# Performance work log

Hardware: AMD Instinct MI355X
Metric: run time of the kernel (lower is better)

## Reference

```python
import jax, jax.numpy as jnp
import numpy as np

D_MODEL = 1024
N_HEADS = 16
N_GROUPS = 4
CONTEXT_LEN = 512
D_H = D_MODEL // N_HEADS          # 64
GROUP_SIZE = N_HEADS // N_GROUPS  # 4
B, S = 4, 2048


def setup_inputs() -> dict:
    key = jax.random.key(0)
    ks = jax.random.split(key, 9)
    s = 0.02
    return {
        "x": jax.random.normal(ks[0], (B, S, D_MODEL), dtype=jnp.float32),
        "Wq": jax.random.normal(ks[1], (D_MODEL, D_MODEL), dtype=jnp.float32) * s,
        "bq": jax.random.normal(ks[2], (D_MODEL,), dtype=jnp.float32) * s,
        "Wk": jax.random.normal(ks[3], (D_MODEL, N_GROUPS * D_H), dtype=jnp.float32) * s,
        "bk": jax.random.normal(ks[4], (N_GROUPS * D_H,), dtype=jnp.float32) * s,
        "Wv": jax.random.normal(ks[5], (D_MODEL, N_GROUPS * D_H), dtype=jnp.float32) * s,
        "bv": jax.random.normal(ks[6], (N_GROUPS * D_H,), dtype=jnp.float32) * s,
        "Wo": jax.random.normal(ks[7], (D_MODEL, D_MODEL), dtype=jnp.float32) * s,
        "bo": jax.random.normal(ks[8], (D_MODEL,), dtype=jnp.float32) * s,
    }


def reference(x, Wq, bq, Wk, bk, Wv, bv, Wo, bo):
    b, s = x.shape[0], x.shape[1]
    # Projections. q: [b, n_groups, group_size, s, d_h]; k/v: [b, n_groups, s, d_h]
    q = (x @ Wq + bq).reshape(b, s, N_GROUPS, GROUP_SIZE, D_H)
    q = jnp.transpose(q, (0, 2, 3, 1, 4))
    k = jnp.transpose((x @ Wk + bk).reshape(b, s, N_GROUPS, D_H), (0, 2, 1, 3))
    v = jnp.transpose((x @ Wv + bv).reshape(b, s, N_GROUPS, D_H), (0, 2, 1, 3))
    # Grouped scores (einsum broadcast == repeat_interleave of k over group_size)
    scores = jnp.einsum("bghqd,bgkd->bghqk", q, k) / jnp.sqrt(jnp.float32(D_H))
    # Sliding-window causal mask (cached_len == s when use_cache=False)
    i = jnp.arange(s)
    j = jnp.arange(s)
    upper = (i - CONTEXT_LEN)[:, None] >= j[None, :]   # too-old keys
    lower = i[:, None] < j[None, :]                    # future keys
    mask = upper | lower                               # [s, s]
    scores = jnp.where(mask, jnp.float32(-1e9), scores)
    att = jax.nn.softmax(scores, axis=-1)
    out = jnp.einsum("bghqk,bgkd->bghqd", att, v)      # [b, g, h, s, d_h]
    out = jnp.transpose(out, (0, 3, 1, 2, 4)).reshape(b, s, D_MODEL)
    return out @ Wo + bo
```

## Files before the change

kernel.cpp:

```cpp
#include <hip/hip_runtime.h>
#include <cstdint>
#include <cstddef>

typedef __attribute__((ext_vector_type(8))) short short8;
typedef __attribute__((ext_vector_type(4))) short short4v;
typedef __attribute__((ext_vector_type(4))) float f32x4;
typedef __attribute__((ext_vector_type(4))) unsigned short ushort4v;
typedef unsigned short ushort_t;

union PFrag { unsigned int w[4]; short8 v; };

__device__ __forceinline__ ushort_t f2bf(float f) {
  unsigned int u = __builtin_bit_cast(unsigned int, f);
  u += 0x7FFFu + ((u >> 16) & 1u);
  return (ushort_t)(u >> 16);
}

__device__ __forceinline__ void gload16(const void* g, void* l) {
  __builtin_amdgcn_global_load_lds(
      (const __attribute__((address_space(1))) unsigned int*)g,
      (__attribute__((address_space(3))) unsigned int*)l, 16, 0, 0);
}

__global__ __launch_bounds__(256) void prep_kernel(
    const float* __restrict__ x, ushort_t* __restrict__ xb,
    const float* __restrict__ Wq, const float* __restrict__ Wk,
    const float* __restrict__ Wv, const float* __restrict__ Wo,
    const float* __restrict__ bq, const float* __restrict__ bk,
    const float* __restrict__ bv, ushort_t* __restrict__ Wt,
    float* __restrict__ bqkv) {
  __shared__ float tile[32][33];
  const int t = threadIdx.x;
  if (blockIdx.x < 8192) {
    const int i = (blockIdx.x * 256 + t) * 4;
    const float4 v = *reinterpret_cast<const float4*>(x + i);
    ushort4v r = { f2bf(v.x), f2bf(v.y), f2bf(v.z), f2bf(v.w) };
    *reinterpret_cast<ushort4v*>(xb + i) = r;
    return;
  }
  const int bid = blockIdx.x - 8192;
  const int tn = bid % 80, tk = bid / 80;
  if (tk == 0) {
    const int u = tn * 256 + t;
    if (u < 1536) bqkv[u] = (u < 1024) ? bq[u] : (u < 1280) ? bk[u - 1024] : bv[u - 1280];
  }
  const int n0 = tn * 32;
  const float* W; int ldn, nloc;
  if      (n0 < 1024) { W = Wq; ldn = 1024; nloc = n0; }
  else if (n0 < 1280) { W = Wk; ldn = 256;  nloc = n0 - 1024; }
  else if (n0 < 1536) { W = Wv; ldn = 256;  nloc = n0 - 1280; }
  else                { W = Wo; ldn = 1024; nloc = n0 - 1536; }
  const int sr = t >> 3, sc = (t & 7) * 4;
  const float4 v = *reinterpret_cast<const float4*>(W + (size_t)(tk * 32 + sr) * ldn + nloc + sc);
  tile[sr][sc] = v.x; tile[sr][sc + 1] = v.y; tile[sr][sc + 2] = v.z; tile[sr][sc + 3] = v.w;
  __syncthreads();
  const int wr = t >> 3, wc = (t & 7) * 4;
  ushort4v o = { f2bf(tile[wc][wr]), f2bf(tile[wc + 1][wr]),
                 f2bf(tile[wc + 2][wr]), f2bf(tile[wc + 3][wr]) };
  *reinterpret_cast<ushort4v*>(Wt + (size_t)(n0 + wr) * 1024 + tk * 32 + wc) = o;
}

#define GEMM_IDS \
  const int tid = threadIdx.x;                        \
  const int w = tid >> 6, lane = tid & 63;            \
  const int wm = w >> 1, wn = w & 1;                  \
  const int g = lane >> 4, r16 = lane & 15;

#define GEMM_KLOOP(APTR, BPTR)                                                          \
  const f32x4 vzero = {0.f, 0.f, 0.f, 0.f};                                             \
  f32x4 acc[4][4];                                                                      \
  _Pragma("unroll") for (int i = 0; i < 4; ++i)                                         \
    _Pragma("unroll") for (int j = 0; j < 4; ++j) acc[i][j] = vzero;                    \
  auto stage = [&](int s, int k0) {                                                     \
    char* base = LdsB + s * 16384;                                                      \
    _Pragma("unroll") for (int i = 0; i < 2; ++i) {                                     \
      const int u = tid + i * 256;                                                      \
      const int row = u >> 2;                                                           \
      const int pu = (u & 3) ^ ((u >> 3) & 3);                                          \
      gload16((const char*)(APTR) + (size_t)(bm * 128 + row) * 2048 + k0 * 2 + pu * 16, \
              base + u * 16);                                                           \
    }                                                                                   \
    _Pragma("unroll") for (int i = 0; i < 2; ++i) {                                     \
      const int u = tid + i * 256;                                                      \
      const int row = u >> 2;                                                           \
      const int pu = (u & 3) ^ ((u >> 3) & 3);                                          \
      gload16((const char*)(BPTR) + (size_t)(bn * 128 + row) * 2048 + k0 * 2 + pu * 16, \
              base + 8192 + u * 16);                                                    \
    }                                                                                   \
  };                                                                                    \
  stage(0, 0);                                                                          \
  stage(1, 32);                                                                         \
  stage(2, 64);                                                                         \
  const int fsw = (g ^ ((r16 >> 1) & 3)) << 4;                                          \
  for (int t = 0; t < 32; ++t) {                                                        \
    if (t < 30)      { asm volatile("s_waitcnt vmcnt(8) lgkmcnt(0)" ::: "memory"); }    \
    else if (t == 30){ asm volatile("s_waitcnt vmcnt(4) lgkmcnt(0)" ::: "memory"); }    \
    else             { asm volatile("s_waitcnt vmcnt(0) lgkmcnt(0)" ::: "memory"); }    \
    __builtin_amdgcn_s_barrier();                                                       \
    if (t + 3 < 32) stage((t + 3) & 3, (t + 3) * 32);                                   \
    const char* Ab = LdsB + (t & 3) * 16384;                                            \
    const char* Bb = Ab + 8192;                                                         \
    short8 af[4], bf[4];                                                                \
    _Pragma("unroll") for (int mi = 0; mi < 4; ++mi)                                    \
      af[mi] = *(const short8*)(Ab + (wm * 64 + mi * 16 + r16) * 64 + fsw);             \
    _Pragma("unroll") for (int ni = 0; ni < 4; ++ni)                                    \
      bf[ni] = *(const short8*)(Bb + (wn * 64 + ni * 16 + r16) * 64 + fsw);             \
    __builtin_amdgcn_s_setprio(1);                                                      \
    _Pragma("unroll") for (int mi = 0; mi < 4; ++mi)                                    \
      _Pragma("unroll") for (int ni = 0; ni < 4; ++ni)                                  \
        acc[mi][ni] = __builtin_amdgcn_mfma_f32_16x16x32_bf16(af[mi], bf[ni], acc[mi][ni], 0, 0, 0); \
    __builtin_amdgcn_s_setprio(0);                                                      \
  }

__global__ __launch_bounds__(256, 2) void gemm_qkv_kernel(
    const ushort_t* __restrict__ A, const ushort_t* __restrict__ Bt,
    const float* __restrict__ bias,
    ushort_t* __restrict__ Qb, ushort_t* __restrict__ Kb, ushort_t* __restrict__ Vt)
{
  __shared__ __align__(16) char LdsB[65536];
  const int xcd = blockIdx.x & 7, ii = blockIdx.x >> 3;
  const int bm = xcd * 8 + ii / 12, bn = ii % 12;
  GEMM_IDS
  GEMM_KLOOP(A, Bt)

  float bcol[4];
#pragma unroll
  for (int ni = 0; ni < 4; ++ni) bcol[ni] = bias[bn * 128 + wn * 64 + ni * 16 + r16];
  if (bn < 8) {
#pragma unroll
    for (int mi = 0; mi < 4; ++mi)
#pragma unroll
      for (int ni = 0; ni < 4; ++ni) {
        const int col = bn * 128 + wn * 64 + ni * 16 + r16;
#pragma unroll
        for (int rr = 0; rr < 4; ++rr) {
          const int row = bm * 128 + wm * 64 + mi * 16 + g * 4 + rr;
          Qb[(size_t)row * 1024 + col] = f2bf((acc[mi][ni][rr] + bcol[ni]) * 0.180336881f);
        }
      }
  } else if (bn < 10) {
#pragma unroll
    for (int mi = 0; mi < 4; ++mi)
#pragma unroll
      for (int ni = 0; ni < 4; ++ni) {
        const int c = bn * 128 + wn * 64 + ni * 16 + r16 - 1024;
        const int gi = c >> 6, dd = c & 63;
#pragma unroll
        for (int rr = 0; rr < 4; ++rr) {
          const int row = bm * 128 + wm * 64 + mi * 16 + g * 4 + rr;
          const int bb = row >> 11, s = row & 2047;
          Kb[((size_t)(bb * 4 + gi) * 2048 + s) * 64 + dd] = f2bf(acc[mi][ni][rr] + bcol[ni]);
        }
      }
  } else {
#pragma unroll
    for (int mi = 0; mi < 4; ++mi) {
      const int row0 = bm * 128 + wm * 64 + mi * 16 + g * 4;
      const int bb = row0 >> 11;
      const int s = row0 & 2047;
      const int pos = (s & ~31) + g * 8 + (mi & 1) * 4;
#pragma unroll
      for (int ni = 0; ni < 4; ++ni) {
        const int c = bn * 128 + wn * 64 + ni * 16 + r16 - 1280;
        const int gi = c >> 6, dd = c & 63;
        ushort4v pk;
#pragma unroll
        for (int rr = 0; rr < 4; ++rr) pk[rr] = f2bf(acc[mi][ni][rr] + bcol[ni]);
        *reinterpret_cast<ushort4v*>(Vt + ((size_t)(bb * 4 + gi) * 64 + dd) * 2048 + pos) = pk;
      }
    }
  }
}

__global__ __launch_bounds__(256, 2) void gemm_out_kernel(
    const ushort_t* __restrict__ A, const ushort_t* __restrict__ Bt,
    const float* __restrict__ bias, float* __restrict__ Cout)
{
  __shared__ __align__(16) char LdsB[65536];
  const int xcd = blockIdx.x & 7, ii = blockIdx.x >> 3;
  const int bm = xcd * 8 + (ii >> 3), bn = ii & 7;
  GEMM_IDS
  GEMM_KLOOP(A, Bt)

  float bcol[4];
#pragma unroll
  for (int ni = 0; ni < 4; ++ni) bcol[ni] = bias[bn * 128 + wn * 64 + ni * 16 + r16];
#pragma unroll
  for (int mi = 0; mi < 4; ++mi)
#pragma unroll
    for (int ni = 0; ni < 4; ++ni) {
      const int col = bn * 128 + wn * 64 + ni * 16 + r16;
#pragma unroll
      for (int rr = 0; rr < 4; ++rr) {
        const int row = bm * 128 + wm * 64 + mi * 16 + g * 4 + rr;
        Cout[(size_t)row * 1024 + col] = acc[mi][ni][rr] + bcol[ni];
      }
    }
}

__global__ __launch_bounds__(512, 2) void attn_kernel(
    const ushort_t* __restrict__ Qb, const ushort_t* __restrict__ Kb,
    const ushort_t* __restrict__ Vt, ushort_t* __restrict__ attout)
{
  __shared__ __align__(16) char KsB[24576];
  __shared__ __align__(16) char VsB[24576];
  const int fid = blockIdx.x;
  const int lo = fid & 7, hi = fid >> 3;
  const int qt = 15 - (hi & 15);
  const int gb = lo | ((hi >> 4) << 3);
  const int gg = gb & 3, b = gb >> 2;

  const int tid = threadIdx.x;
  const int w = tid >> 6, lane = tid & 63;
  const int g = lane >> 4, r16 = lane & 15;
  const int q0w = qt * 128 + w * 16;

  short8 qf[4][2];
#pragma unroll
  for (int hh = 0; hh < 4; ++hh) {
    const int h = gg * 4 + hh;
    const char* qptr = (const char*)Qb + ((size_t)(b * 2048 + q0w + r16) * 1024 + h * 64) * 2;
#pragma unroll
    for (int dc = 0; dc < 2; ++dc)
      qf[hh][dc] = *(const short8*)(qptr + dc * 64 + g * 16);
  }

  const f32x4 vzero = {0.f, 0.f, 0.f, 0.f};
  f32x4 accO[4][4];
#pragma unroll
  for (int hh = 0; hh < 4; ++hh)
#pragma unroll
    for (int nt = 0; nt < 4; ++nt) accO[hh][nt] = vzero;
  float lsum[4] = {0.f, 0.f, 0.f, 0.f};

  const char* KbB = (const char*)Kb + (size_t)(b * 4 + gg) * 2048 * 128;
  const char* VtB = (const char*)Vt + (size_t)(b * 4 + gg) * 64 * 4096;

  const int kb0 = (qt >= 4) ? (qt * 128 - 512) : 0;
  const int NT = (qt * 128 + 128 - kb0) >> 6;

  const int srr = tid >> 3, spk = tid & 7;
  auto stage = [&](int buf, int kb) {
    gload16(KbB + (size_t)(kb + srr) * 128 + ((spk ^ (srr & 7)) << 4),
            KsB + buf * 8192 + tid * 16);
    gload16(VtB + (size_t)srr * 4096 + (size_t)kb * 2 + ((spk ^ (srr & 7)) << 4),
            VsB + buf * 8192 + tid * 16);
  };

  stage(0, kb0);
  if (NT > 1) stage(1, kb0 + 64);
  for (int t = 0; t < NT; ++t) {
    if (t < NT - 1) { asm volatile("s_waitcnt vmcnt(2) lgkmcnt(0)" ::: "memory"); }
    else            { asm volatile("s_waitcnt vmcnt(0) lgkmcnt(0)" ::: "memory"); }
    __builtin_amdgcn_s_barrier();
    if (t + 2 < NT) stage((t + 2) % 3, kb0 + (t + 2) * 64);
    const int kb = kb0 + t * 64;
    const char* Ks = KsB + (t % 3) * 8192;
    const char* Vs = VsB + (t % 3) * 8192;

    f32x4 st[4][4];
#pragma unroll
    for (int ki = 0; ki < 4; ++ki) {
      const int key = ki * 16 + r16;
      const int swz = key & 7;
      const short8 kf0 = *(const short8*)(Ks + key * 128 + ((g ^ swz) << 4));
      const short8 kf1 = *(const short8*)(Ks + key * 128 + (((4 + g) ^ swz) << 4));
#pragma unroll
      for (int hh = 0; hh < 4; ++hh) {
        st[hh][ki] = __builtin_amdgcn_mfma_f32_16x16x32_bf16(kf0, qf[hh][0], vzero, 0, 0, 0);
        st[hh][ki] = __builtin_amdgcn_mfma_f32_16x16x32_bf16(kf1, qf[hh][1], st[hh][ki], 0, 0, 0);
      }
    }

    const bool full = (kb >= q0w - 496) && (kb <= q0w - 63);
    if (full) {
#pragma unroll
      for (int hh = 0; hh < 4; ++hh)
#pragma unroll
        for (int ki = 0; ki < 4; ++ki)
#pragma unroll
          for (int r = 0; r < 4; ++r)
            st[hh][ki][r] = __builtin_amdgcn_exp2f(st[hh][ki][r]);
    } else {
      const int q = q0w + r16;
#pragma unroll
      for (int ki = 0; ki < 4; ++ki)
#pragma unroll
        for (int r = 0; r < 4; ++r) {
          const int key = kb + ki * 16 + g * 4 + r;
          const bool valid = (key <= q) && (key + 512 > q);
#pragma unroll
          for (int hh = 0; hh < 4; ++hh)
            st[hh][ki][r] = __builtin_amdgcn_exp2f(valid ? st[hh][ki][r] : -INFINITY);
        }
    }
    PFrag pf[4][2];
#pragma unroll
    for (int hh = 0; hh < 4; ++hh) {
      float tk[4];
#pragma unroll
      for (int ki = 0; ki < 4; ++ki)
        tk[ki] = (st[hh][ki][0] + st[hh][ki][1]) + (st[hh][ki][2] + st[hh][ki][3]);
      lsum[hh] += (tk[0] + tk[1]) + (tk[2] + tk[3]);
#pragma unroll
      for (int c = 0; c < 2; ++c)
#pragma unroll
        for (int pr = 0; pr < 2; ++pr) {
          asm("v_cvt_pk_bf16_f32 %0, %1, %2"
              : "=v"(pf[hh][c].w[pr * 2])
              : "v"(st[hh][2 * c + pr][0]), "v"(st[hh][2 * c + pr][1]));
          asm("v_cvt_pk_bf16_f32 %0, %1, %2"
              : "=v"(pf[hh][c].w[pr * 2 + 1])
              : "v"(st[hh][2 * c + pr][2]), "v"(st[hh][2 * c + pr][3]));
        }
    }

#pragma unroll
    for (int c = 0; c < 2; ++c)
#pragma unroll
      for (int nt = 0; nt < 4; ++nt) {
        const int d = nt * 16 + r16;
        const short8 vf = *(const short8*)(Vs + d * 128 + (((c * 4 + g) ^ (d & 7)) << 4));
#pragma unroll
        for (int hh = 0; hh < 4; ++hh)
          accO[hh][nt] = __builtin_amdgcn_mfma_f32_16x16x32_bf16(pf[hh][c].v, vf, accO[hh][nt], 0, 0, 0);
      }
  }

#pragma unroll
  for (int hh = 0; hh < 4; ++hh) {
    float ts = lsum[hh];
    ts += __shfl_xor(ts, 16);
    ts += __shfl_xor(ts, 32);
    const float linv = 1.f / ts;
    float lq[4];
#pragma unroll
    for (int rr = 0; rr < 4; ++rr) lq[rr] = __shfl(linv, g * 4 + rr);
    const int h = gg * 4 + hh;
#pragma unroll
    for (int nt = 0; nt < 4; ++nt) {
      const int ocol = h * 64 + nt * 16 + r16;
#pragma unroll
      for (int rr = 0; rr < 4; ++rr) {
        const int orow = b * 2048 + q0w + g * 4 + rr;
        attout[(size_t)orow * 1024 + ocol] = f2bf(accO[hh][nt][rr] * lq[rr]);
      }
    }
  }
}

extern "C" void kernel_launch(void* const* d_in, const int* in_sizes, int n_in,
                              void* d_out, int out_size, void* d_ws, size_t ws_size,
                              hipStream_t stream) {
  (void)in_sizes; (void)n_in; (void)out_size; (void)ws_size;
  const float* x  = (const float*)d_in[0];
  const float* Wq = (const float*)d_in[1];
  const float* bq = (const float*)d_in[2];
  const float* Wk = (const float*)d_in[3];
  const float* bk = (const float*)d_in[4];
  const float* Wv = (const float*)d_in[5];
  const float* bv = (const float*)d_in[6];
  const float* Wo = (const float*)d_in[7];
  const float* bo = (const float*)d_in[8];

  char* ws = (char*)d_ws;
  ushort_t* Qb   = (ushort_t*)(ws + 0);
  ushort_t* Kb   = (ushort_t*)(ws + 16777216);
  ushort_t* Vt   = (ushort_t*)(ws + 20971520);
  ushort_t* wt   = (ushort_t*)(ws + 25165824);
  float*    bqkv = (float*)   (ws + 30408704);
  ushort_t* xb   = (ushort_t*)(ws + 30416896);
  ushort_t* att  = (ushort_t*)(ws + 47194112);

  prep_kernel<<<10752, 256, 0, stream>>>(x, xb, Wq, Wk, Wv, Wo, bq, bk, bv, wt, bqkv);
  gemm_qkv_kernel<<<768, 256, 0, stream>>>(xb, wt, bqkv, Qb, Kb, Vt);
  attn_kernel<<<256, 512, 0, stream>>>(Qb, Kb, Vt, att);
  gemm_out_kernel<<<512, 256, 0, stream>>>(att, wt + (size_t)1536 * 1024, bo, (float*)d_out);
}
```

Before: 102.7 us.

## Use 256x256 tiles with 512 threads for QKV GEMM; triple-buffer out GEMM

The QKV projection GEMM moves from 128x128 tiles with 256 threads and a 4-stage pipeline to 256x256 tiles with 512 threads (8 waves), a 128-wide K step, double buffering and an XOR-swizzled LDS layout. The larger tiles raise data reuse per block and cut global traffic, but the grid drops to 192 blocks on a GPU with more CUs than that, leaving some idle. The output GEMM goes from 4 to 3 LDS stages so three blocks can share a CU, which trades prefetch depth for occupancy.

```diff
diff --git a/kernel.cpp b/kernel.cpp
--- a/kernel.cpp
+++ b/kernel.cpp
@@ -60,127 +60,204 @@
   *reinterpret_cast<ushort4v*>(Wt + (size_t)(n0 + wr) * 1024 + tk * 32 + wc) = o;
 }
 
+__global__ __launch_bounds__(512) void gemm_qkv_kernel(
+    const ushort_t* __restrict__ A, const ushort_t* __restrict__ Bt,
+    const float* __restrict__ bias,
+    ushort_t* __restrict__ Qb, ushort_t* __restrict__ Kb, ushort_t* __restrict__ Vt)
+{
+  __shared__ __align__(16) char LdsB[131072];
+  const int xcd = blockIdx.x & 7, ii = blockIdx.x >> 3;
+  const int bm = xcd * 4 + ii / 6, bn = ii % 6;
+  const int tid = threadIdx.x;
+  const int w = tid >> 6, lane = tid & 63;
+  const int wm = w >> 2, wn = w & 3;
+  const int g = lane >> 4, r16 = lane & 15;
+
+  const f32x4 vzero = {0.f, 0.f, 0.f, 0.f};
+  f32x4 acc[8][4];
+#pragma unroll
+  for (int i = 0; i < 8; ++i)
+#pragma unroll
+    for (int j = 0; j < 4; ++j) acc[i][j] = vzero;
+
+  auto stage = [&](int s, int kt) {
+#pragma unroll
+    for (int i = 0; i < 4; ++i) {
+      const int u = tid + i * 512;
+      const int row = u >> 3, phys = u & 7;
+      gload16((const char*)A + (size_t)(bm * 256 + row) * 2048 + kt * 128
+                  + ((phys ^ (row & 7)) << 4),
+              LdsB + s * 32768 + u * 16);
+    }
+#pragma unroll
+    for (int i = 0; i < 4; ++i) {
+      const int u = tid + i * 512;
+      const int row = u >> 3, phys = u & 7;
+      gload16((const char*)Bt + (size_t)(bn * 256 + row) * 2048 + kt * 128
+                  + ((phys ^ (row & 7)) << 4),
+              LdsB + 65536 + s * 32768 + u * 16);
+    }
+  };
+
+  stage(0, 0);
+  asm volatile("s_waitcnt vmcnt(0)" ::: "memory");
+  __builtin_amdgcn_s_barrier();
+
+  for (int kt = 0; kt < 16; ++kt) {
+    const int s = kt & 1;
+    if (kt + 1 < 16) stage(s ^ 1, kt + 1);
+    const char* Ab = LdsB + s * 32768;
+    const char* Bb = LdsB + 65536 + s * 32768;
+#pragma unroll
+    for (int q = 0; q < 4; ++q) {
+      const int mh = q >> 1, nh = q & 1;
+      short8 af[4][2], bf[2][2];
+#pragma unroll
+      for (int m = 0; m < 4; ++m) {
+        const int row = wm * 128 + (mh * 4 + m) * 16 + r16;
+#pragma unroll
+        for (int kc = 0; kc < 2; ++kc)
+          af[m][kc] = *(const short8*)(Ab + row * 128 + (((kc * 4 + g) ^ (row & 7)) << 4));
+      }
+#pragma unroll
+      for (int n = 0; n < 2; ++n) {
+        const int row = wn * 64 + (nh * 2 + n) * 16 + r16;
+#pragma unroll
+        for (int kc = 0; kc < 2; ++kc)
+          bf[n][kc] = *(const short8*)(Bb + row * 128 + (((kc * 4 + g) ^ (row & 7)) << 4));
+      }
+      __builtin_amdgcn_s_setprio(1);
+#pragma unroll
+      for (int m = 0; m < 4; ++m)
+#pragma unroll
+        for (int n = 0; n < 2; ++n)
+#pragma unroll
+          for (int kc = 0; kc < 2; ++kc)
+            acc[mh * 4 + m][nh * 2 + n] = __builtin_amdgcn_mfma_f32_16x16x32_bf16(
+                af[m][kc], bf[n][kc], acc[mh * 4 + m][nh * 2 + n], 0, 0, 0);
+      __builtin_amdgcn_s_setprio(0);
+      __builtin_amdgcn_s_barrier();
+    }
+    if (kt + 1 < 16) { asm volatile("s_waitcnt vmcnt(0)" ::: "memory"); }
+    __builtin_amdgcn_s_barrier();
+  }
+
+  float bcol[4];
+#pragma unroll
+  for (int ni = 0; ni < 4; ++ni) bcol[ni] = bias[bn * 256 + wn * 64 + ni * 16 + r16];
+  if (bn < 4) {
+#pragma unroll
+    for (int mi = 0; mi < 8; ++mi)
+#pragma unroll
+      for (int ni = 0; ni < 4; ++ni) {
+        const int col = bn * 256 + wn * 64 + ni * 16 + r16;
+#pragma unroll
+        for (int rr = 0; rr < 4; ++rr) {
+          const int row = bm * 256 + wm * 128 + mi * 16 + g * 4 + rr;
+          Qb[(size_t)row * 1024 + col] = f2bf((acc[mi][ni][rr] + bcol[ni]) * 0.180336881f);
+        }
+      }
+  } else if (bn == 4) {
+    const int dd = wn * 0 + 0 + (0);
+    (void)dd;
+#pragma unroll
+    for (int mi = 0; mi < 8; ++mi)
+#pragma unroll
+      for (int ni = 0; ni < 4; ++ni) {
+        const int c = wn * 64 + ni * 16 + r16;
+        const int gi = c >> 6, d2 = c & 63;
+#pragma unroll
+        for (int rr = 0; rr < 4; ++rr) {
+          const int row = bm * 256 + wm * 128 + mi * 16 + g * 4 + rr;
+          const int bb = row >> 11, sR = row & 2047;
+          Kb[((size_t)(bb * 4 + gi) * 2048 + sR) * 64 + d2] = f2bf(acc[mi][ni][rr] + bcol[ni]);
+        }
+      }
+  } else {
+#pragma unroll
+    for (int mi = 0; mi < 8; ++mi) {
+      const int row0 = bm * 256 + wm * 128 + mi * 16 + g * 4;
+      const int bb = row0 >> 11;
+      const int sR = row0 & 2047;
+      const int pos = (sR & ~31) + g * 8 + (mi & 1) * 4;
+#pragma unroll
+      for (int ni = 0; ni < 4; ++ni) {
+        const int c = wn * 64 + ni * 16 + r16;
+        const int gi = c >> 6, d2 = c & 63;
+        ushort4v pk;
+#pragma unroll
+        for (int rr = 0; rr < 4; ++rr) pk[rr] = f2bf(acc[mi][ni][rr] + bcol[ni]);
+        *reinterpret_cast<ushort4v*>(Vt + ((size_t)(bb * 4 + gi) * 64 + d2) * 2048 + pos) = pk;
+      }
+    }
+  }
+}
+
 #define GEMM_IDS \
   const int tid = threadIdx.x;                        \
   const int w = tid >> 6, lane = tid & 63;            \
   const int wm = w >> 1, wn = w & 1;                  \
   const int g = lane >> 4, r16 = lane & 15;
 
-#define GEMM_KLOOP(APTR, BPTR)                                                          \
-  const f32x4 vzero = {0.f, 0.f, 0.f, 0.f};                                             \
-  f32x4 acc[4][4];                                                                      \
-  _Pragma("unroll") for (int i = 0; i < 4; ++i)                                         \
-    _Pragma("unroll") for (int j = 0; j < 4; ++j) acc[i][j] = vzero;                    \
-  auto stage = [&](int s, int k0) {                                                     \
-    char* base = LdsB + s * 16384;                                                      \
-    _Pragma("unroll") for (int i = 0; i < 2; ++i) {                                     \
-      const int u = tid + i * 256;                                                      \
-      const int row = u >> 2;                                                           \
-      const int pu = (u & 3) ^ ((u >> 3) & 3);                                          \
-      gload16((const char*)(APTR) + (size_t)(bm * 128 + row) * 2048 + k0 * 2 + pu * 16, \
-              base + u * 16);                                                           \
-    }                                                                                   \
-    _Pragma("unroll") for (int i = 0; i < 2; ++i) {                                     \
-      const int u = tid + i * 256;                                                      \
-      const int row = u >> 2;                                                           \
-      const int pu = (u & 3) ^ ((u >> 3) & 3);                                          \
-      gload16((const char*)(BPTR) + (size_t)(bn * 128 + row) * 2048 + k0 * 2 + pu * 16, \
-              base + 8192 + u * 16);                                                    \
-    }                                                                                   \
-  };                                                                                    \
-  stage(0, 0);                                                                          \
-  stage(1, 32);                                                                         \
-  stage(2, 64);                                                                         \
-  const int fsw = (g ^ ((r16 >> 1) & 3)) << 4;                                          \
-  for (int t = 0; t < 32; ++t) {                                                        \
-    if (t < 30)      { asm volatile("s_waitcnt vmcnt(8) lgkmcnt(0)" ::: "memory"); }    \
-    else if (t == 30){ asm volatile("s_waitcnt vmcnt(4) lgkmcnt(0)" ::: "memory"); }    \
-    else             { asm volatile("s_waitcnt vmcnt(0) lgkmcnt(0)" ::: "memory"); }    \
-    __builtin_amdgcn_s_barrier();                                                       \
-    if (t + 3 < 32) stage((t + 3) & 3, (t + 3) * 32);                                   \
-    const char* Ab = LdsB + (t & 3) * 16384;                                            \
-    const char* Bb = Ab + 8192;                                                         \
-    short8 af[4], bf[4];                                                                \
-    _Pragma("unroll") for (int mi = 0; mi < 4; ++mi)                                    \
-      af[mi] = *(const short8*)(Ab + (wm * 64 + mi * 16 + r16) * 64 + fsw);             \
-    _Pragma("unroll") for (int ni = 0; ni < 4; ++ni)                                    \
-      bf[ni] = *(const short8*)(Bb + (wn * 64 + ni * 16 + r16) * 64 + fsw);             \
-    __builtin_amdgcn_s_setprio(1);                                                      \
-    _Pragma("unroll") for (int mi = 0; mi < 4; ++mi)                                    \
-      _Pragma("unroll") for (int ni = 0; ni < 4; ++ni)                                  \
-        acc[mi][ni] = __builtin_amdgcn_mfma_f32_16x16x32_bf16(af[mi], bf[ni], acc[mi][ni], 0, 0, 0); \
-    __builtin_amdgcn_s_setprio(0);                                                      \
-  }
-
-__global__ __launch_bounds__(256, 2) void gemm_qkv_kernel(
-    const ushort_t* __restrict__ A, const ushort_t* __restrict__ Bt,
-    const float* __restrict__ bias,
-    ushort_t* __restrict__ Qb, ushort_t* __restrict__ Kb, ushort_t* __restrict__ Vt)
-{
-  __shared__ __align__(16) char LdsB[65536];
-  const int xcd = blockIdx.x & 7, ii = blockIdx.x >> 3;
-  const int bm = xcd * 8 + ii / 12, bn = ii % 12;
-  GEMM_IDS
-  GEMM_KLOOP(A, Bt)
-
-  float bcol[4];
-#pragma unroll
-  for (int ni = 0; ni < 4; ++ni) bcol[ni] = bias[bn * 128 + wn * 64 + ni * 16 + r16];
-  if (bn < 8) {
-#pragma unroll
-    for (int mi = 0; mi < 4; ++mi)
-#pragma unroll
-      for (int ni = 0; ni < 4; ++ni) {
-        const int col = bn * 128 + wn * 64 + ni * 16 + r16;
-#pragma unroll
-        for (int rr = 0; rr < 4; ++rr) {
-          const int row = bm * 128 + wm * 64 + mi * 16 + g * 4 + rr;
-          Qb[(size_t)row * 1024 + col] = f2bf((acc[mi][ni][rr] + bcol[ni]) * 0.180336881f);
-        }
-      }
-  } else if (bn < 10) {
-#pragma unroll
-    for (int mi = 0; mi < 4; ++mi)
-#pragma unroll
-      for (int ni = 0; ni < 4; ++ni) {
-        const int c = bn * 128 + wn * 64 + ni * 16 + r16 - 1024;
-        const int gi = c >> 6, dd = c & 63;
-#pragma unroll
-        for (int rr = 0; rr < 4; ++rr) {
-          const int row = bm * 128 + wm * 64 + mi * 16 + g * 4 + rr;
-          const int bb = row >> 11, s = row & 2047;
-          Kb[((size_t)(bb * 4 + gi) * 2048 + s) * 64 + dd] = f2bf(acc[mi][ni][rr] + bcol[ni]);
-        }
-      }
-  } else {
-#pragma unroll
-    for (int mi = 0; mi < 4; ++mi) {
-      const int row0 = bm * 128 + wm * 64 + mi * 16 + g * 4;
-      const int bb = row0 >> 11;
-      const int s = row0 & 2047;
-      const int pos = (s & ~31) + g * 8 + (mi & 1) * 4;
-#pragma unroll
-      for (int ni = 0; ni < 4; ++ni) {
-        const int c = bn * 128 + wn * 64 + ni * 16 + r16 - 1280;
-        const int gi = c >> 6, dd = c & 63;
-        ushort4v pk;
-#pragma unroll
-        for (int rr = 0; rr < 4; ++rr) pk[rr] = f2bf(acc[mi][ni][rr] + bcol[ni]);
-        *reinterpret_cast<ushort4v*>(Vt + ((size_t)(bb * 4 + gi) * 64 + dd) * 2048 + pos) = pk;
-      }
-    }
-  }
-}
-
-__global__ __launch_bounds__(256, 2) void gemm_out_kernel(
+__global__ __launch_bounds__(256, 3) void gemm_out_kernel(
     const ushort_t* __restrict__ A, const ushort_t* __restrict__ Bt,
     const float* __restrict__ bias, float* __restrict__ Cout)
 {
-  __shared__ __align__(16) char LdsB[65536];
+  __shared__ __align__(16) char LdsB[49152];
   const int xcd = blockIdx.x & 7, ii = blockIdx.x >> 3;
   const int bm = xcd * 8 + (ii >> 3), bn = ii & 7;
   GEMM_IDS
-  GEMM_KLOOP(A, Bt)
+
+  const f32x4 vzero = {0.f, 0.f, 0.f, 0.f};
+  f32x4 acc[4][4];
+#pragma unroll
+  for (int i = 0; i < 4; ++i)
+#pragma unroll
+    for (int j = 0; j < 4; ++j) acc[i][j] = vzero;
+  auto stage = [&](int s, int k0) {
+    char* base = LdsB + s * 16384;
+#pragma unroll
+    for (int i = 0; i < 2; ++i) {
+      const int u = tid + i * 256;
+      const int row = u >> 2;
+      const int pu = (u & 3) ^ ((u >> 3) & 3);
+      gload16((const char*)A + (size_t)(bm * 128 + row) * 2048 + k0 * 2 + pu * 16,
+              base + u * 16);
+    }
+#pragma unroll
+    for (int i = 0; i < 2; ++i) {
+      const int u = tid + i * 256;
+      const int row = u >> 2;
+      const int pu = (u & 3) ^ ((u >> 3) & 3);
+      gload16((const char*)Bt + (size_t)(bn * 128 + row) * 2048 + k0 * 2 + pu * 16,
+              base + 8192 + u * 16);
+    }
+  };
+  stage(0, 0);
+  stage(1, 32);
+  const int fsw = (g ^ ((r16 >> 1) & 3)) << 4;
+  for (int t = 0; t < 32; ++t) {
+    if (t < 31) { asm volatile("s_waitcnt vmcnt(4) lgkmcnt(0)" ::: "memory"); }
+    else        { asm volatile("s_waitcnt vmcnt(0) lgkmcnt(0)" ::: "memory"); }
+    __builtin_amdgcn_s_barrier();
+    if (t + 2 < 32) stage((t + 2) % 3, (t + 2) * 32);
+    const char* Ab = LdsB + (t % 3) * 16384;
+    const char* Bb = Ab + 8192;
+    short8 af[4], bf[4];
+#pragma unroll
+    for (int mi = 0; mi < 4; ++mi)
+      af[mi] = *(const short8*)(Ab + (wm * 64 + mi * 16 + r16) * 64 + fsw);
+#pragma unroll
+    for (int ni = 0; ni < 4; ++ni)
+      bf[ni] = *(const short8*)(Bb + (wn * 64 + ni * 16 + r16) * 64 + fsw);
+    __builtin_amdgcn_s_setprio(1);
+#pragma unroll
+    for (int mi = 0; mi < 4; ++mi)
+#pragma unroll
+      for (int ni = 0; ni < 4; ++ni)
+        acc[mi][ni] = __builtin_amdgcn_mfma_f32_16x16x32_bf16(af[mi], bf[ni], acc[mi][ni], 0, 0, 0);
+    __builtin_amdgcn_s_setprio(0);
+  }
 
   float bcol[4];
 #pragma unroll
@@ -373,7 +450,7 @@
   ushort_t* att  = (ushort_t*)(ws + 47194112);
 
   prep_kernel<<<10752, 256, 0, stream>>>(x, xb, Wq, Wk, Wv, Wo, bq, bk, bv, wt, bqkv);
-  gemm_qkv_kernel<<<768, 256, 0, stream>>>(xb, wt, bqkv, Qb, Kb, Vt);
+  gemm_qkv_kernel<<<192, 512, 0, stream>>>(xb, wt, bqkv, Qb, Kb, Vt);
   attn_kernel<<<256, 512, 0, stream>>>(Qb, Kb, Vt, att);
   gemm_out_kernel<<<512, 256, 0, stream>>>(att, wt + (size_t)1536 * 1024, bo, (float*)d_out);
 }
```

New measurement: 103.3 us. Within noise of the previous version (+0.6%).
